# Optimization experiments

Hardware: AMD Instinct MI355X
Metric: run time of the kernel (lower is better)

Reference implementation:

```python
import jax, jax.numpy as jnp
import numpy as np

NUM_HEADS = 12
ROPE_THETA = 10000.0


def rope_angles(hd, end_x, end_y):
    # axial 2D rope angles, shape (L, hd//2); first hd//4 from x-coord, next hd//4 from y-coord
    f = 1.0 / (ROPE_THETA ** (np.arange(0, hd, 4)[: hd // 4].astype(np.float32) / hd))
    t = np.arange(end_x * end_y)
    tx = (t % end_x).astype(np.float32)
    ty = (t // end_x).astype(np.float32)
    ang = np.concatenate([np.outer(tx, f), np.outer(ty, f)], axis=-1)
    return jnp.asarray(ang, dtype=jnp.float32)


def apply_rope(q, ang):
    # q: (B, nH, L, hd); complex multiply on adjacent pairs
    cos, sin = jnp.cos(ang), jnp.sin(ang)  # (L, hd//2)
    qr = q.reshape(*q.shape[:-1], -1, 2)
    a, b = qr[..., 0], qr[..., 1]
    return jnp.stack([a * cos - b * sin, a * sin + b * cos], axis=-1).reshape(q.shape)


def setup_inputs() -> dict:
    key = jax.random.key(0)
    ks = jax.random.split(key, 7)
    dim, H, W, B = 768, 32, 32, 8
    hd = dim // NUM_HEADS
    return {
        "x": jax.random.normal(ks[0], (B, H, W, dim), jnp.float32),
        "qkv_w": jax.random.normal(ks[1], (3 * dim, dim), jnp.float32) * 0.02,
        "qkv_b": jax.random.normal(ks[2], (3 * dim,), jnp.float32) * 0.02,
        "proj_w": jax.random.normal(ks[3], (dim, dim), jnp.float32) * 0.02,
        "proj_b": jax.random.normal(ks[4], (dim,), jnp.float32) * 0.02,
        "rel_pos_h": jax.random.normal(ks[5], (2 * H - 1, hd), jnp.float32) * 0.02,
        "rel_pos_w": jax.random.normal(ks[6], (2 * W - 1, hd), jnp.float32) * 0.02,
    }


def reference(x, qkv_w, qkv_b, proj_w, proj_b, rel_pos_h, rel_pos_w):
    B, H, W, dim = x.shape
    nH = NUM_HEADS
    hd = dim // nH
    L = H * W
    qkv = jnp.einsum("blc,dc->bld", x.reshape(B, L, dim), qkv_w) + qkv_b
    qkv = qkv.reshape(B, L, 3, nH, hd)
    q = qkv[:, :, 0].transpose(0, 2, 1, 3)  # (B, nH, L, hd)
    k = qkv[:, :, 1].transpose(0, 2, 1, 3)
    v = qkv[:, :, 2].transpose(0, 2, 1, 3)
    # 2D rope (applied to both q and k)
    ang = rope_angles(hd, H, W)
    q = apply_rope(q, ang)
    k = apply_rope(k, ang)
    # relative position bias: equivalent math of concat_rel_pos(rescale=True) + SDPA
    # effective scores = (q.k)/sqrt(hd) + rel_h + rel_w
    rc = jnp.arange(H)[:, None] - jnp.arange(W)[None, :] + (H - 1)  # (H, W)
    Rh = rel_pos_h[rc]  # (H, K_h, hd)
    Rw = rel_pos_w[rc]  # (W, K_w, hd)
    rq = q.reshape(B, nH, H, W, hd)
    rel_h = jnp.einsum("bnhwc,hkc->bnhwk", rq, Rh)  # (B, nH, H, W, K_h)
    rel_w = jnp.einsum("bnhwc,wkc->bnhwk", rq, Rw)  # (B, nH, H, W, K_w)
    scores = jnp.einsum("bnqc,bnkc->bnqk", q, k) / jnp.sqrt(jnp.float32(hd))
    scores = scores.reshape(B, nH, H, W, H, W) + rel_h[..., :, None] + rel_w[..., None, :]
    attn = jax.nn.softmax(scores.reshape(B, nH, L, L), axis=-1)
    out = jnp.einsum("bnqk,bnkc->bnqc", attn, v)  # (B, nH, L, hd)
    out = out.transpose(0, 2, 1, 3).reshape(B, H, W, dim)
    return jnp.einsum("bhwc,dc->bhwd", out, proj_w) + proj_b
```

## Files before the change

kernel.cpp:

```cpp
#include <hip/hip_runtime.h>


typedef unsigned short u16;
typedef __attribute__((ext_vector_type(8))) __bf16 bf16x8;
typedef __attribute__((ext_vector_type(4))) float f32x4;
typedef __attribute__((address_space(1))) const unsigned int gu32;
typedef __attribute__((address_space(3))) unsigned int lu32;

#define LOG2E 1.4426950408889634f

__device__ __forceinline__ float b2f(u16 u) {
    unsigned int i = ((unsigned int)u) << 16;
    float f; __builtin_memcpy(&f, &i, 4); return f;
}
__device__ __forceinline__ u16 f2b(float f) {
    unsigned int x; __builtin_memcpy(&x, &f, 4);
    x += 0x7fffu + ((x >> 16) & 1u);
    return (u16)(x >> 16);
}

#define LDT 72

__global__ void detect_dtype(const u16* __restrict__ x, int* __restrict__ flag)
{
    if (threadIdx.x == 0 && blockIdx.x == 0) {
        float mx = 0.f;
        for (int i = 0; i < 128; i++) {
            float v = fabsf(b2f(x[i]));
            if (!(v <= 1e30f)) v = 1e30f;
            mx = fmaxf(mx, v);
        }
        *flag = (mx > 1e4f) ? 1 : 0;
    }
}

struct CvtArgs {
    const void* src[7];
    u16*        dst[7];
    int         n[7];
    float       sc[7];
};

__global__ __launch_bounds__(256) void convert_all(CvtArgs a, const int* __restrict__ flag)
{
    const int fl = *flag;
    const int g = blockIdx.x * 256 + threadIdx.x;
    const int stride = gridDim.x * 256;
    #pragma unroll 1
    for (int s = 0; s < 7; s++) {
        const int n = a.n[s];
        const float sc = a.sc[s];
        const float* fs = (const float*)a.src[s];
        const u16*  hs = (const u16*)a.src[s];
        u16* d = a.dst[s];
        for (int i = g; i < n; i += stride) {
            float v = fl ? fs[i] : b2f(hs[i]);
            d[i] = f2b(v * sc);
        }
    }
}

template <int EPI>
__global__ __launch_bounds__(256) void gemm128(
    const u16* __restrict__ A, const u16* __restrict__ Bw,
    const u16* __restrict__ bias, void* __restrict__ Cout,
    const int* __restrict__ flag, u16* __restrict__ qkvT, int N, int K)
{
    __shared__ __align__(16) u16 smem[16384];
    u16* lA = smem;
    u16* lB = smem + 8192;
    u16* ct = smem;
    const int tid = threadIdx.x;
    const int m0 = blockIdx.x * 128, n0 = blockIdx.y * 128;
    const int wave = tid >> 6, lane = tid & 63;
    const int wm = (wave & 1) * 64, wn = (wave >> 1) * 64;
    const int lm = lane & 15, lq = lane >> 4;
    const int srow = lane >> 3, scol = (lane & 7) * 8;
    f32x4 acc[4][4] = {};
    for (int k0 = 0; k0 < K; k0 += 64) {
        if (k0) __syncthreads();
        #pragma unroll
        for (int c4 = 0; c4 < 4; c4++) {
            const int c = wave * 4 + c4;
            const int row = c * 8 + srow;
            __builtin_amdgcn_global_load_lds(
                (gu32*)(A + (size_t)(m0 + row) * K + k0 + scol),
                (lu32*)&lA[c * 512], 16, 0, 0);
            __builtin_amdgcn_global_load_lds(
                (gu32*)(Bw + (size_t)(n0 + row) * K + k0 + scol),
                (lu32*)&lB[c * 512], 16, 0, 0);
        }
        __syncthreads();
        #pragma unroll
        for (int ks = 0; ks < 64; ks += 32) {
            bf16x8 af[4], bfr[4];
            #pragma unroll
            for (int i = 0; i < 4; i++) af[i]  = *(const bf16x8*)&lA[(wm + i * 16 + lm) * 64 + ks + lq * 8];
            #pragma unroll
            for (int j = 0; j < 4; j++) bfr[j] = *(const bf16x8*)&lB[(wn + j * 16 + lm) * 64 + ks + lq * 8];
            #pragma unroll
            for (int i = 0; i < 4; i++)
                #pragma unroll
                for (int j = 0; j < 4; j++)
                    acc[i][j] = __builtin_amdgcn_mfma_f32_16x16x32_bf16(af[i], bfr[j], acc[i][j], 0, 0, 0);
        }
    }
    if (EPI == 0) {
        const int fl = *flag;
        #pragma unroll
        for (int j = 0; j < 4; j++) {
            const int n = n0 + wn + j * 16 + lm;
            const float bj = b2f(bias[n]);
            #pragma unroll
            for (int i = 0; i < 4; i++)
                #pragma unroll
                for (int r = 0; r < 4; r++) {
                    const int m = m0 + wm + i * 16 + lq * 4 + r;
                    const float v = acc[i][j][r] + bj;
                    if (fl) ((float*)Cout)[(size_t)m * 768 + n] = v;
                    else    ((u16*)Cout)[(size_t)m * 768 + n] = f2b(v);
                }
        }
    } else {
        const int which = n0 / 768;
        const bool vt = (which == 2);
        __syncthreads();
        #pragma unroll
        for (int j = 0; j < 4; j++) {
            const int nl = wn + j * 16 + lm;
            const int n = n0 + nl;
            const float bj = b2f(bias[n]);
            #pragma unroll
            for (int i = 0; i < 4; i++)
                #pragma unroll
                for (int r = 0; r < 4; r++) {
                    const int ml = wm + i * 16 + lq * 4 + r;
                    const int m = m0 + ml;
                    float v = acc[i][j][r] + bj;
                    const float p = __shfl_xor(v, 1);
                    const int l = m & 1023, d = n & 63;
                    float o = v;
                    if (which < 2) {
                        const int pi = d >> 1, jj = pi & 15;
                        const float coord = (pi < 16) ? (float)(l & 31) : (float)(l >> 5);
                        const float ang = coord * __expf(-(float)jj * 0.5756462732485115f);
                        float sn, cs; __sincosf(ang, &sn, &cs);
                        o = v * cs + ((d & 1) ? p * sn : -(p * sn));
                        if (which == 1) o *= 0.125f * LOG2E;
                    }
                    ct[vt ? nl * 128 + ml : ml * 128 + nl] = f2b(o);
                }
        }
        __syncthreads();
        const size_t HL = (size_t)96 * 1024 * 64;
        const int nh0 = (n0 >> 6) % 12, bb = m0 >> 10, l0 = m0 & 1023;
        if (!vt) {
            #pragma unroll
            for (int pass = 0; pass < 8; pass++) {
                const int chunk = pass * 256 + tid;
                const int run = chunk >> 3, lc = chunk & 7;
                const int ml = run >> 1, h = run & 1;
                u16* gp = qkvT + (size_t)which * HL
                        + ((size_t)(bb * 12 + nh0 + h) * 1024 + l0 + ml) * 64 + lc * 8;
                *(uint4*)gp = *(const uint4*)&ct[ml * 128 + h * 64 + lc * 8];
            }
        } else {
            const int kt0 = l0 >> 6;
            #pragma unroll
            for (int pass = 0; pass < 8; pass++) {
                const int run = pass * 16 + (tid >> 4);
                const int ln = tid & 15;
                const int half = ln >> 3, l8 = ln & 7;
                u16* gp = qkvT + 2 * HL
                        + (size_t)(bb * 12 + nh0 + (run >> 6)) * 65536
                        + (size_t)(kt0 + half) * 4096 + (run & 63) * 64 + l8 * 8;
                *(uint4*)gp = *(const uint4*)&ct[run * 128 + ln * 8];
            }
        }
    }
}

__global__ __launch_bounds__(256) void flash_attn_mfma(
    const u16* __restrict__ qkvT, const u16* __restrict__ relH,
    const u16* __restrict__ relW, u16* __restrict__ outb)
{
    __shared__ __align__(16) u16 ks2[64 * 64];
    __shared__ __align__(16) u16 vsT[64 * 64];
    __shared__ __align__(16) u16 qs[64 * LDT];
    __shared__ __align__(16) u16 Th[64 * LDT];
    __shared__ __align__(16) u16 Tw[64 * LDT];
    u16* rel = vsT;
    u16* pT  = qs;

    const int tid = threadIdx.x;
    const int bn = blockIdx.x, q0 = blockIdx.y * 64;
    const size_t HL = (size_t)96 * 1024 * 64;
    const u16* qg  = qkvT + (size_t)bn * 65536 + (size_t)q0 * 64;
    const u16* kgb = qkvT + HL + (size_t)bn * 65536;
    const u16* vgb = qkvT + 2 * HL + (size_t)bn * 65536;

    for (int g = tid; g < 1024; g += 256) {
        int r = g >> 4, c = (g & 15) * 4;
        *(ushort4*)&qs[r * LDT + c] = ((const ushort4*)qg)[g];
    }
    for (int g = tid; g < 1008; g += 256) {
        int r = g >> 4, c = (g & 15) * 4;
        *(ushort4*)&rel[r * 64 + c] = *(const ushort4*)(relH + g * 4);
    }
    if (tid < 16) { ushort4 z = {0, 0, 0, 0}; *(ushort4*)&rel[63 * 64 + tid * 4] = z; }
    __syncthreads();

    const int w = tid >> 6, lane = tid & 63;
    const int lm = lane & 15, lq = lane >> 4;

    const bf16x8 bq0 = *(const bf16x8*)&qs[(w * 16 + lm) * LDT + lq * 8];
    const bf16x8 bq1 = *(const bf16x8*)&qs[(w * 16 + lm) * LDT + 32 + lq * 8];

    {
        f32x4 tacc[4] = {};
        #pragma unroll
        for (int nb = 0; nb < 4; nb++) {
            bf16x8 r0 = *(const bf16x8*)&rel[(nb * 16 + lm) * 64 + lq * 8];
            bf16x8 r1 = *(const bf16x8*)&rel[(nb * 16 + lm) * 64 + 32 + lq * 8];
            tacc[nb] = __builtin_amdgcn_mfma_f32_16x16x32_bf16(bq0, r0, tacc[nb], 0, 0, 0);
            tacc[nb] = __builtin_amdgcn_mfma_f32_16x16x32_bf16(bq1, r1, tacc[nb], 0, 0, 0);
        }
        #pragma unroll
        for (int nb = 0; nb < 4; nb++)
            #pragma unroll
            for (int rr = 0; rr < 4; rr++)
                Th[(w * 16 + lq * 4 + rr) * LDT + nb * 16 + lm] = f2b(tacc[nb][rr]);
    }
    __syncthreads();
    for (int g = tid; g < 1008; g += 256) {
        int r = g >> 4, c = (g & 15) * 4;
        *(ushort4*)&rel[r * 64 + c] = *(const ushort4*)(relW + g * 4);
    }
    if (tid < 16) { ushort4 z = {0, 0, 0, 0}; *(ushort4*)&rel[63 * 64 + tid * 4] = z; }
    __syncthreads();
    {
        f32x4 tacc[4] = {};
        #pragma unroll
        for (int nb = 0; nb < 4; nb++) {
            bf16x8 r0 = *(const bf16x8*)&rel[(nb * 16 + lm) * 64 + lq * 8];
            bf16x8 r1 = *(const bf16x8*)&rel[(nb * 16 + lm) * 64 + 32 + lq * 8];
            tacc[nb] = __builtin_amdgcn_mfma_f32_16x16x32_bf16(bq0, r0, tacc[nb], 0, 0, 0);
            tacc[nb] = __builtin_amdgcn_mfma_f32_16x16x32_bf16(bq1, r1, tacc[nb], 0, 0, 0);
        }
        #pragma unroll
        for (int nb = 0; nb < 4; nb++)
            #pragma unroll
            for (int rr = 0; rr < 4; rr++)
                Tw[(w * 16 + lq * 4 + rr) * LDT + nb * 16 + lm] = f2b(tacc[nb][rr]);
    }
    const int qw = (w & 1) * 16 + lm;
    float rwc[8];
    #pragma unroll
    for (int mb2 = 0; mb2 < 2; mb2++)
        #pragma unroll
        for (int rr = 0; rr < 4; rr++) {
            const int kw = mb2 * 16 + lq * 4 + rr;
            rwc[mb2 * 4 + rr] = b2f(Tw[(w * 16 + lm) * LDT + qw - kw + 31]) - 16.0f;
        }
    const int qh = (q0 >> 5) + (w >= 2 ? 1 : 0);

    const int srow = lane >> 3, scol = (lane & 7) * 8;
    float l_acc = 0.f;
    f32x4 oacc[4] = {};

    #pragma unroll 1
    for (int kt = 0; kt < 16; kt++) {
        __syncthreads();
        const u16* kp = kgb + (size_t)kt * 4096;
        const u16* vp = vgb + (size_t)kt * 4096;
        #pragma unroll
        for (int c4 = 0; c4 < 2; c4++) {
            const int c = w * 2 + c4;
            const int row = c * 8 + srow;
            __builtin_amdgcn_global_load_lds(
                (gu32*)(kp + row * 64 + scol), (lu32*)&ks2[c * 512], 16, 0, 0);
            __builtin_amdgcn_global_load_lds(
                (gu32*)(vp + row * 64 + scol), (lu32*)&vsT[c * 512], 16, 0, 0);
        }
        __syncthreads();
        f32x4 sacc[4];
        #pragma unroll
        for (int mb = 0; mb < 4; mb++) {
            bf16x8 ka0 = *(const bf16x8*)&ks2[(mb * 16 + lm) * 64 + lq * 8];
            bf16x8 ka1 = *(const bf16x8*)&ks2[(mb * 16 + lm) * 64 + 32 + lq * 8];
            f32x4 s = {};
            s = __builtin_amdgcn_mfma_f32_16x16x32_bf16(ka0, bq0, s, 0, 0, 0);
            s = __builtin_amdgcn_mfma_f32_16x16x32_bf16(ka1, bq1, s, 0, 0, 0);
            sacc[mb] = s;
        }
        const float rh0 = b2f(Th[(w * 16 + lm) * LDT + qh - 2 * kt + 31]);
        const float rh1 = b2f(Th[(w * 16 + lm) * LDT + qh - 2 * kt + 30]);
        #pragma unroll
        for (int mb = 0; mb < 4; mb++) {
            const float rhv = (mb >= 2) ? rh1 : rh0;
            unsigned pk[2];
            #pragma unroll
            for (int h = 0; h < 2; h++) {
                float p0 = exp2f(sacc[mb][2 * h]     + rhv + rwc[(mb & 1) * 4 + 2 * h]);
                float p1 = exp2f(sacc[mb][2 * h + 1] + rhv + rwc[(mb & 1) * 4 + 2 * h + 1]);
                l_acc += p0; l_acc += p1;
                unsigned u0, u1;
                __builtin_memcpy(&u0, &p0, 4); __builtin_memcpy(&u1, &p1, 4);
                pk[h] = __builtin_amdgcn_perm(u1 + 0x8000u, u0 + 0x8000u, 0x07060302u);
            }
            uint2 u = {pk[0], pk[1]};
            *(uint2*)&pT[(w * 16 + lm) * LDT + mb * 16 + lq * 4] = u;
        }
        const bf16x8 pa0 = *(const bf16x8*)&pT[(w * 16 + lm) * LDT + lq * 8];
        const bf16x8 pa1 = *(const bf16x8*)&pT[(w * 16 + lm) * LDT + 32 + lq * 8];
        #pragma unroll
        for (int nb = 0; nb < 4; nb++) {
            bf16x8 vb0 = *(const bf16x8*)&vsT[(nb * 16 + lm) * 64 + lq * 8];
            bf16x8 vb1 = *(const bf16x8*)&vsT[(nb * 16 + lm) * 64 + 32 + lq * 8];
            oacc[nb] = __builtin_amdgcn_mfma_f32_16x16x32_bf16(pa0, vb0, oacc[nb], 0, 0, 0);
            oacc[nb] = __builtin_amdgcn_mfma_f32_16x16x32_bf16(pa1, vb1, oacc[nb], 0, 0, 0);
        }
    }
    l_acc += __shfl_xor(l_acc, 16);
    l_acc += __shfl_xor(l_acc, 32);
    const float rinv = 1.f / l_acc;
    float rv[4];
    #pragma unroll
    for (int rr = 0; rr < 4; rr++) rv[rr] = __shfl(rinv, lq * 4 + rr);
    const int bb = bn / 12, nh = bn % 12;
    #pragma unroll
    for (int nb = 0; nb < 4; nb++)
        #pragma unroll
        for (int rr = 0; rr < 4; rr++) {
            const int qrow = q0 + w * 16 + lq * 4 + rr;
            const int d = nb * 16 + lm;
            outb[((size_t)(bb * 1024 + qrow)) * 768 + nh * 64 + d] = f2b(oacc[nb][rr] * rv[rr]);
        }
}

extern "C" void kernel_launch(void* const* d_in, const int* in_sizes, int n_in,
                              void* d_out, int out_size, void* d_ws, size_t ws_size,
                              hipStream_t stream)
{
    u16* ws16  = (u16*)d_ws;
    u16* qkvT  = ws16;
    u16* xb    = ws16 + (size_t)18874368;
    u16* attn  = xb;
    const size_t S = 25165824;
    u16* qkvw_b = ws16 + S;
    u16* projw_b = qkvw_b + 1769472;
    u16* qkvb_b = projw_b + 589824;
    u16* projb_b = qkvb_b + 2304;
    u16* relh_b = projb_b + 768;
    u16* relw_b = relh_b + 4032;
    int* flag = (int*)(ws16 + S + 2370432);

    detect_dtype<<<1, 64, 0, stream>>>((const u16*)d_in[0], flag);

    CvtArgs ca;
    ca.src[0] = d_in[0]; ca.dst[0] = xb;      ca.n[0] = 6291456; ca.sc[0] = 1.0f;
    ca.src[1] = d_in[1]; ca.dst[1] = qkvw_b;  ca.n[1] = 1769472; ca.sc[1] = 1.0f;
    ca.src[2] = d_in[3]; ca.dst[2] = projw_b; ca.n[2] = 589824;  ca.sc[2] = 1.0f;
    ca.src[3] = d_in[2]; ca.dst[3] = qkvb_b;  ca.n[3] = 2304;    ca.sc[3] = 1.0f;
    ca.src[4] = d_in[4]; ca.dst[4] = projb_b; ca.n[4] = 768;     ca.sc[4] = 1.0f;
    ca.src[5] = d_in[5]; ca.dst[5] = relh_b;  ca.n[5] = 4032;    ca.sc[5] = LOG2E;
    ca.src[6] = d_in[6]; ca.dst[6] = relw_b;  ca.n[6] = 4032;    ca.sc[6] = LOG2E;
    convert_all<<<2048, 256, 0, stream>>>(ca, flag);

    gemm128<1><<<dim3(64, 18), 256, 0, stream>>>(xb, qkvw_b, qkvb_b, nullptr, flag, qkvT, 2304, 768);
    flash_attn_mfma<<<dim3(96, 16), 256, 0, stream>>>(qkvT, relh_b, relw_b, attn);
    gemm128<0><<<dim3(64, 6), 256, 0, stream>>>(attn, projw_b, projb_b, d_out, flag, nullptr, 768, 768);
}
```

Measured before the change: 269.5 us.

## Double-buffer K/V tiles in flash attention and XOR-swizzle LDS layouts

The attention kernel now keeps two LDS buffers each for K and V. It prefetches the next key tile with async global-to-LDS loads while the current tile is being computed, and drops one barrier per iteration. Both the GEMM and the attention kernel XOR-swizzle the 16-byte chunk column by the row index when loading, and apply the matching swizzle when reading MFMA fragments, to cut LDS bank conflicts. This uses more shared memory in the attention kernel, which could lower occupancy.

```diff
diff --git a/kernel.cpp b/kernel.cpp
--- a/kernel.cpp
+++ b/kernel.cpp
@@ -75,7 +75,10 @@
     const int wave = tid >> 6, lane = tid & 63;
     const int wm = (wave & 1) * 64, wn = (wave >> 1) * 64;
     const int lm = lane & 15, lq = lane >> 4;
-    const int srow = lane >> 3, scol = (lane & 7) * 8;
+    const int srow = lane >> 3;
+    const int sgcol = ((lane & 7) ^ (srow & 7)) * 8;
+    const int sw0 = (lq ^ (lm & 7)) * 8;
+    const int sw1 = ((lq + 4) ^ (lm & 7)) * 8;
     f32x4 acc[4][4] = {};
     for (int k0 = 0; k0 < K; k0 += 64) {
         if (k0) __syncthreads();
@@ -84,20 +87,21 @@
             const int c = wave * 4 + c4;
             const int row = c * 8 + srow;
             __builtin_amdgcn_global_load_lds(
-                (gu32*)(A + (size_t)(m0 + row) * K + k0 + scol),
+                (gu32*)(A + (size_t)(m0 + row) * K + k0 + sgcol),
                 (lu32*)&lA[c * 512], 16, 0, 0);
             __builtin_amdgcn_global_load_lds(
-                (gu32*)(Bw + (size_t)(n0 + row) * K + k0 + scol),
+                (gu32*)(Bw + (size_t)(n0 + row) * K + k0 + sgcol),
                 (lu32*)&lB[c * 512], 16, 0, 0);
         }
         __syncthreads();
         #pragma unroll
         for (int ks = 0; ks < 64; ks += 32) {
+            const int sw = ks ? sw1 : sw0;
             bf16x8 af[4], bfr[4];
             #pragma unroll
-            for (int i = 0; i < 4; i++) af[i]  = *(const bf16x8*)&lA[(wm + i * 16 + lm) * 64 + ks + lq * 8];
-            #pragma unroll
-            for (int j = 0; j < 4; j++) bfr[j] = *(const bf16x8*)&lB[(wn + j * 16 + lm) * 64 + ks + lq * 8];
+            for (int i = 0; i < 4; i++) af[i]  = *(const bf16x8*)&lA[(wm + i * 16 + lm) * 64 + sw];
+            #pragma unroll
+            for (int j = 0; j < 4; j++) bfr[j] = *(const bf16x8*)&lB[(wn + j * 16 + lm) * 64 + sw];
             #pragma unroll
             for (int i = 0; i < 4; i++)
                 #pragma unroll
@@ -184,8 +188,8 @@
     const u16* __restrict__ qkvT, const u16* __restrict__ relH,
     const u16* __restrict__ relW, u16* __restrict__ outb)
 {
-    __shared__ __align__(16) u16 ks2[64 * 64];
-    __shared__ __align__(16) u16 vsT[64 * 64];
+    __shared__ __align__(16) u16 ks2[2 * 4096];
+    __shared__ __align__(16) u16 vsT[2 * 4096];
     __shared__ __align__(16) u16 qs[64 * LDT];
     __shared__ __align__(16) u16 Th[64 * LDT];
     __shared__ __align__(16) u16 Tw[64 * LDT];
@@ -264,30 +268,47 @@
         }
     const int qh = (q0 >> 5) + (w >= 2 ? 1 : 0);
 
-    const int srow = lane >> 3, scol = (lane & 7) * 8;
+    const int srow = lane >> 3;
+    const int sgcol = ((lane & 7) ^ (srow & 7)) * 8;
+    const int sw0 = (lq ^ (lm & 7)) * 8;
+    const int sw1 = ((lq + 4) ^ (lm & 7)) * 8;
     float l_acc = 0.f;
     f32x4 oacc[4] = {};
+
+    __syncthreads();
+    #pragma unroll
+    for (int c4 = 0; c4 < 2; c4++) {
+        const int c = w * 2 + c4;
+        const int row = c * 8 + srow;
+        __builtin_amdgcn_global_load_lds(
+            (gu32*)(kgb + row * 64 + sgcol), (lu32*)&ks2[c * 512], 16, 0, 0);
+        __builtin_amdgcn_global_load_lds(
+            (gu32*)(vgb + row * 64 + sgcol), (lu32*)&vsT[c * 512], 16, 0, 0);
+    }
 
     #pragma unroll 1
     for (int kt = 0; kt < 16; kt++) {
         __syncthreads();
-        const u16* kp = kgb + (size_t)kt * 4096;
-        const u16* vp = vgb + (size_t)kt * 4096;
-        #pragma unroll
-        for (int c4 = 0; c4 < 2; c4++) {
-            const int c = w * 2 + c4;
-            const int row = c * 8 + srow;
-            __builtin_amdgcn_global_load_lds(
-                (gu32*)(kp + row * 64 + scol), (lu32*)&ks2[c * 512], 16, 0, 0);
-            __builtin_amdgcn_global_load_lds(
-                (gu32*)(vp + row * 64 + scol), (lu32*)&vsT[c * 512], 16, 0, 0);
-        }
-        __syncthreads();
+        const int bo = (kt & 1) * 4096;
+        if (kt < 15) {
+            const int bn1 = ((kt + 1) & 1) * 4096;
+            const u16* kp = kgb + (size_t)(kt + 1) * 4096;
+            const u16* vp = vgb + (size_t)(kt + 1) * 4096;
+            #pragma unroll
+            for (int c4 = 0; c4 < 2; c4++) {
+                const int c = w * 2 + c4;
+                const int row = c * 8 + srow;
+                __builtin_amdgcn_global_load_lds(
+                    (gu32*)(kp + row * 64 + sgcol), (lu32*)&ks2[bn1 + c * 512], 16, 0, 0);
+                __builtin_amdgcn_global_load_lds(
+                    (gu32*)(vp + row * 64 + sgcol), (lu32*)&vsT[bn1 + c * 512], 16, 0, 0);
+            }
+        }
         f32x4 sacc[4];
         #pragma unroll
         for (int mb = 0; mb < 4; mb++) {
-            bf16x8 ka0 = *(const bf16x8*)&ks2[(mb * 16 + lm) * 64 + lq * 8];
-            bf16x8 ka1 = *(const bf16x8*)&ks2[(mb * 16 + lm) * 64 + 32 + lq * 8];
+            bf16x8 ka0 = *(const bf16x8*)&ks2[bo + (mb * 16 + lm) * 64 + sw0];
+            bf16x8 ka1 = *(const bf16x8*)&ks2[bo + (mb * 16 + lm) * 64 + sw1];
             f32x4 s = {};
             s = __builtin_amdgcn_mfma_f32_16x16x32_bf16(ka0, bq0, s, 0, 0, 0);
             s = __builtin_amdgcn_mfma_f32_16x16x32_bf16(ka1, bq1, s, 0, 0, 0);
@@ -315,8 +336,8 @@
         const bf16x8 pa1 = *(const bf16x8*)&pT[(w * 16 + lm) * LDT + 32 + lq * 8];
         #pragma unroll
         for (int nb = 0; nb < 4; nb++) {
-            bf16x8 vb0 = *(const bf16x8*)&vsT[(nb * 16 + lm) * 64 + lq * 8];
-            bf16x8 vb1 = *(const bf16x8*)&vsT[(nb * 16 + lm) * 64 + 32 + lq * 8];
+            bf16x8 vb0 = *(const bf16x8*)&vsT[bo + (nb * 16 + lm) * 64 + sw0];
+            bf16x8 vb1 = *(const bf16x8*)&vsT[bo + (nb * 16 + lm) * 64 + sw1];
             oacc[nb] = __builtin_amdgcn_mfma_f32_16x16x32_bf16(pa0, vb0, oacc[nb], 0, 0, 0);
             oacc[nb] = __builtin_amdgcn_mfma_f32_16x16x32_bf16(pa1, vb1, oacc[nb], 0, 0, 0);
         }
```

Result: faster. 249.3 us (-7.5%).
